# Kernel tuning notes

Measured on AMD Instinct MI355X. Metric: run time of the kernel, lower is better.

The kernel has to match this reference:

```python
import jax, jax.numpy as jnp
import numpy as np

N_DIM = 16
E_DIM = 16
M_DIM = 16
HIDDEN = 64
N_EDGE = 1_600_000
N_NODE = 100_000


def setup_inputs() -> dict:
    key = jax.random.key(0)
    k1, k2, k3, k4, k5, k6, k7 = jax.random.split(key, 7)
    index_v = jax.random.randint(k1, (N_EDGE,), 0, N_NODE, dtype=jnp.int32)
    h_w = jax.random.normal(k2, (N_EDGE, N_DIM), dtype=jnp.float32)
    e_vw = jax.random.normal(k3, (N_EDGE, E_DIM), dtype=jnp.float32)
    # NNet params: Linear(e_dim, hidden) -> ReLU -> Linear(hidden, n_dim*m_dim)
    s1 = 1.0 / np.sqrt(E_DIM)
    s2 = 1.0 / np.sqrt(HIDDEN)
    W1 = jax.random.uniform(k4, (E_DIM, HIDDEN), jnp.float32, -s1, s1)
    b1 = jax.random.uniform(k5, (HIDDEN,), jnp.float32, -s1, s1)
    W2 = jax.random.uniform(k6, (HIDDEN, N_DIM * M_DIM), jnp.float32, -s2, s2)
    b2 = jax.random.uniform(k7, (N_DIM * M_DIM,), jnp.float32, -s2, s2)
    return {"index_v": index_v, "h_w": h_w, "e_vw": e_vw, "n_node": N_NODE,
            "W1": W1, "b1": b1, "W2": W2, "b2": b2}


def reference(index_v, h_w, e_vw, n_node, W1, b1, W2, b2):
    # Edge MLP: [n_edge, e_dim] -> [n_edge, n_dim*m_dim]
    hid = jax.nn.relu(e_vw @ W1 + b1)
    A_vw = (hid @ W2 + b2).reshape(-1, M_DIM, N_DIM)  # [n_edge, m_dim, n_dim]
    # Per-edge matvec: bmm(A_vw, h_w[:, :, None]) -> [n_edge, m_dim]
    m_vw = jnp.einsum("emn,en->em", A_vw, h_w)
    # Scatter-add messages to target nodes: [n_node, m_dim]
    m_v = jax.ops.segment_sum(m_vw, index_v, num_segments=n_node)
    return m_v
```

## Files before the change

### kernel.cpp

```cpp
#include <hip/hip_runtime.h>
#include <stdint.h>

typedef __bf16 bf16x8 __attribute__((ext_vector_type(8)));
typedef float  f32x4  __attribute__((ext_vector_type(4)));
typedef float  fvec4  __attribute__((ext_vector_type(4)));
typedef float  f32x2  __attribute__((ext_vector_type(2)));

#define EDIM   16
#define HIDDEN 64
#define MDIM   16
#define NDIM   16
#define KCHUNKS 32
#define NREP   8
#define WPB    8

__device__ __forceinline__ uint32_t pack_trunc(float x, float y) {
    return __builtin_amdgcn_perm(__builtin_bit_cast(uint32_t, x),
                                 __builtin_bit_cast(uint32_t, y),
                                 0x03020706u);
}

__device__ __forceinline__ uint16_t f32_to_bf16_rne(float f) {
    uint32_t u = __builtin_bit_cast(uint32_t, f);
    u += 0x7FFFu + ((u >> 16) & 1u);
    return (uint16_t)(u >> 16);
}

__device__ __forceinline__ bf16x8 u4_as_bf16x8(uint32_t a, uint32_t b,
                                               uint32_t c, uint32_t d) {
    union { uint32_t u[4]; bf16x8 v; } x;
    x.u[0] = a; x.u[1] = b; x.u[2] = c; x.u[3] = d;
    return x.v;
}

__device__ __forceinline__ f32x2 pk_mul(f32x2 a, f32x2 b) {
    f32x2 d;
    asm("v_pk_mul_f32 %0, %1, %2" : "=v"(d) : "v"(a), "v"(b));
    return d;
}

__device__ __forceinline__ void atomic_add_s(const float* base, uint32_t off,
                                             float v) {
    asm volatile("global_atomic_add_f32 %0, %1, %2"
                 :: "v"(off), "v"(v), "s"(base) : "memory");
}

template<int REPL>
__global__ __launch_bounds__(512, 6) void msg_mfma(
    const int*   __restrict__ idx,
    const float* __restrict__ h_w,
    const float* __restrict__ e_vw,
    const float* __restrict__ W1,
    const float* __restrict__ b1,
    const float* __restrict__ W2,
    const float* __restrict__ b2,
    float*       __restrict__ outb,
    int n_edge, int rep_stride)
{
    __align__(16) __shared__ ushort sB[KCHUNKS * 512];
    __align__(16) __shared__ ushort sHid[WPB * 64 * 16];

    const int tid = threadIdx.x;

    const float* out;
    if (REPL) {
        int xcd = __builtin_amdgcn_s_getreg(6164) & (NREP - 1);
        out = outb + (size_t)xcd * (size_t)rep_stride;
    } else {
        out = outb;
    }

    for (int t = tid; t < KCHUNKS * 512; t += 512) {
        int c = t >> 9, r = t & 511;
        int qq = r >> 7, m = (r >> 3) & 15, j = r & 7;
        int k = 2 * c + (qq >> 1);
        int n = ((qq & 1) << 3) + j;
        sB[t] = f32_to_bf16_rne(W2[k * 256 + m * 16 + n]);
    }

    const int lane = tid & 63;
    const int q    = lane >> 4;
    const int col  = lane & 15;
    const int w    = tid >> 6;

    uint32_t w1u[4][4];
    #pragma unroll
    for (int nt = 0; nt < 4; nt++) {
        #pragma unroll
        for (int d = 0; d < 4; d++) w1u[nt][d] = 0;
        #pragma unroll
        for (int j = 0; j < 8; j++) {
            int k = q * 8 + j;
            float v = 0.f;
            if (k < 16)       v = W1[k * 64 + nt * 16 + col];
            else if (k == 16) v = b1[nt * 16 + col];
            w1u[nt][j >> 1] |= ((uint32_t)f32_to_bf16_rne(v)) << ((j & 1) * 16);
        }
    }

    uint32_t b2u[4] = {0, 0, 0, 0};
    if (q < 2) {
        const float* bp = b2 + col * 16 + q * 8;
        #pragma unroll
        for (int j = 0; j < 8; j++)
            b2u[j >> 1] |= ((uint32_t)f32_to_bf16_rne(bp[j])) << ((j & 1) * 16);
    }
    __syncthreads();

    bf16x8 w1f[4];
    #pragma unroll
    for (int nt = 0; nt < 4; nt++)
        w1f[nt] = u4_as_bf16x8(w1u[nt][0], w1u[nt][1], w1u[nt][2], w1u[nt][3]);
    const bf16x8 b2f = u4_as_bf16x8(b2u[0], b2u[1], b2u[2], b2u[3]);

    const int nhalf = (q & 1) << 3;
    const int ntile = (n_edge + 15) >> 4;
    const int wave_id = blockIdx.x * WPB + w;
    const int wstride = gridDim.x * WPB;
    if (wave_id >= ntile) return;

    const ushort* hidRd = &sHid[w * 1024 + (q >> 1) * 16 + col];
    ushort*       hidWr = &sHid[w * 1024 + col * 16 + q * 4];
    const ushort* bRd   = &sB[q * 128 + col * 8];
    const uint32_t col4 = (uint32_t)col * 4u;

    int t = wave_id;
    fvec4 e0, e1, h0, h1; int4 nd; bool full;
    {
        int rbase = t * 16;
        full = (rbase + 16 <= n_edge);
        int row = full ? (rbase + col) : min(rbase + col, n_edge - 1);
        uint32_t ro = (uint32_t)row * 16u + (uint32_t)nhalf;
        const fvec4* ep = (const fvec4*)(e_vw + ro);
        e0 = __builtin_nontemporal_load(ep);
        e1 = __builtin_nontemporal_load(ep + 1);
        const fvec4* hp = (const fvec4*)(h_w + ro);
        h0 = __builtin_nontemporal_load(hp);
        h1 = __builtin_nontemporal_load(hp + 1);
        int r0 = rbase + q * 4;
        if (full) {
            nd.x = __builtin_nontemporal_load(idx + r0 + 0);
            nd.y = __builtin_nontemporal_load(idx + r0 + 1);
            nd.z = __builtin_nontemporal_load(idx + r0 + 2);
            nd.w = __builtin_nontemporal_load(idx + r0 + 3);
        } else {
            nd.x = __builtin_nontemporal_load(idx + min(r0 + 0, n_edge - 1));
            nd.y = __builtin_nontemporal_load(idx + min(r0 + 1, n_edge - 1));
            nd.z = __builtin_nontemporal_load(idx + min(r0 + 2, n_edge - 1));
            nd.w = __builtin_nontemporal_load(idx + min(r0 + 3, n_edge - 1));
        }
    }

    while (true) {
        int tn = t + wstride;
        bool have_next = (tn < ntile);
        fvec4 ne0, ne1, nh0, nh1; int4 nnd; bool nfull = false;
        if (have_next) {
            int rbase = tn * 16;
            nfull = (rbase + 16 <= n_edge);
            int row = nfull ? (rbase + col) : min(rbase + col, n_edge - 1);
            uint32_t ro = (uint32_t)row * 16u + (uint32_t)nhalf;
            const fvec4* ep = (const fvec4*)(e_vw + ro);
            ne0 = __builtin_nontemporal_load(ep);
            ne1 = __builtin_nontemporal_load(ep + 1);
            const fvec4* hp = (const fvec4*)(h_w + ro);
            nh0 = __builtin_nontemporal_load(hp);
            nh1 = __builtin_nontemporal_load(hp + 1);
            int r0 = rbase + q * 4;
            if (nfull) {
                nnd.x = __builtin_nontemporal_load(idx + r0 + 0);
                nnd.y = __builtin_nontemporal_load(idx + r0 + 1);
                nnd.z = __builtin_nontemporal_load(idx + r0 + 2);
                nnd.w = __builtin_nontemporal_load(idx + r0 + 3);
            } else {
                nnd.x = __builtin_nontemporal_load(idx + min(r0 + 0, n_edge - 1));
                nnd.y = __builtin_nontemporal_load(idx + min(r0 + 1, n_edge - 1));
                nnd.z = __builtin_nontemporal_load(idx + min(r0 + 2, n_edge - 1));
                nnd.w = __builtin_nontemporal_load(idx + min(r0 + 3, n_edge - 1));
            }
        }

        uint32_t au0 = pack_trunc(e0.x, e0.y);
        uint32_t au1 = pack_trunc(e0.z, e0.w);
        uint32_t au2 = pack_trunc(e1.x, e1.y);
        uint32_t au3 = pack_trunc(e1.z, e1.w);
        if (q == 2) { au0 = 0x00003F80u; au1 = au2 = au3 = 0; }
        else if (q == 3) { au0 = au1 = au2 = au3 = 0; }
        bf16x8 av = u4_as_bf16x8(au0, au1, au2, au3);

        #pragma unroll
        for (int nt = 0; nt < 4; nt++) {
            f32x4 hc = {0.f, 0.f, 0.f, 0.f};
            hc = __builtin_amdgcn_mfma_f32_16x16x32_bf16(av, w1f[nt], hc, 0, 0, 0);
            uint32_t lo = pack_trunc(fmaxf(hc[0], 0.f), fmaxf(hc[1], 0.f));
            uint32_t hi = pack_trunc(fmaxf(hc[2], 0.f), fmaxf(hc[3], 0.f));
            *(uint2*)(hidWr + nt * 256) = make_uint2(lo, hi);
        }

        f32x2 hp0; hp0.x = h0.x; hp0.y = h0.y;
        f32x2 hp1; hp1.x = h0.z; hp1.y = h0.w;
        f32x2 hp2; hp2.x = h1.x; hp2.y = h1.y;
        f32x2 hp3; hp3.x = h1.z; hp3.y = h1.w;

        f32x4 acc = {0.f, 0.f, 0.f, 0.f};
        {
            uint32_t a0 = pack_trunc(hp0.x, hp0.y);
            uint32_t a1 = pack_trunc(hp1.x, hp1.y);
            uint32_t a2 = pack_trunc(hp2.x, hp2.y);
            uint32_t a3 = pack_trunc(hp3.x, hp3.y);
            bf16x8 af = u4_as_bf16x8(a0, a1, a2, a3);
            acc = __builtin_amdgcn_mfma_f32_16x16x32_bf16(af, b2f, acc, 0, 0, 0);
        }

        #pragma unroll
        for (int c = 0; c < KCHUNKS; c++) {
            uint32_t hku = ((uint32_t)hidRd[c * 32]) << 16;
            float hkf = __builtin_bit_cast(float, hku);
            f32x2 hk2; hk2.x = hkf; hk2.y = hkf;
            f32x2 p0 = pk_mul(hk2, hp0);
            f32x2 p1 = pk_mul(hk2, hp1);
            f32x2 p2 = pk_mul(hk2, hp2);
            f32x2 p3 = pk_mul(hk2, hp3);
            uint32_t a0 = pack_trunc(p0.x, p0.y);
            uint32_t a1 = pack_trunc(p1.x, p1.y);
            uint32_t a2 = pack_trunc(p2.x, p2.y);
            uint32_t a3 = pack_trunc(p3.x, p3.y);
            bf16x8 af = u4_as_bf16x8(a0, a1, a2, a3);
            bf16x8 bfb = *(const bf16x8*)(bRd + c * 512);
            acc = __builtin_amdgcn_mfma_f32_16x16x32_bf16(af, bfb, acc, 0, 0, 0);
        }

        if (REPL) {
            if (full) {
                atomic_add_s(out, (uint32_t)nd.x * 64u + col4, acc[0]);
                atomic_add_s(out, (uint32_t)nd.y * 64u + col4, acc[1]);
                atomic_add_s(out, (uint32_t)nd.z * 64u + col4, acc[2]);
                atomic_add_s(out, (uint32_t)nd.w * 64u + col4, acc[3]);
            } else {
                int r0 = t * 16 + q * 4;
                if (r0 + 0 < n_edge) atomic_add_s(out, (uint32_t)nd.x * 64u + col4, acc[0]);
                if (r0 + 1 < n_edge) atomic_add_s(out, (uint32_t)nd.y * 64u + col4, acc[1]);
                if (r0 + 2 < n_edge) atomic_add_s(out, (uint32_t)nd.z * 64u + col4, acc[2]);
                if (r0 + 3 < n_edge) atomic_add_s(out, (uint32_t)nd.w * 64u + col4, acc[3]);
            }
        } else {
            float* o = (float*)out;
            int r0 = t * 16 + q * 4;
            if (r0 + 0 < n_edge) atomicAdd(o + (size_t)nd.x * 16 + col, acc[0]);
            if (r0 + 1 < n_edge) atomicAdd(o + (size_t)nd.y * 16 + col, acc[1]);
            if (r0 + 2 < n_edge) atomicAdd(o + (size_t)nd.z * 16 + col, acc[2]);
            if (r0 + 3 < n_edge) atomicAdd(o + (size_t)nd.w * 16 + col, acc[3]);
        }

        if (!have_next) break;
        t = tn;
        e0 = ne0; e1 = ne1; h0 = nh0; h1 = nh1; nd = nnd; full = nfull;
    }
}

__global__ void merge_rep(const fvec4* __restrict__ rep,
                          fvec4* __restrict__ out, int n4, int stride4)
{
    int i = blockIdx.x * blockDim.x + threadIdx.x;
    if (i >= n4) return;
    fvec4 s = rep[i];
    #pragma unroll
    for (int r = 1; r < NREP; r++)
        s += rep[(size_t)r * stride4 + i];
    out[i] = s;
}

extern "C" void kernel_launch(void* const* d_in, const int* in_sizes, int n_in,
                              void* d_out, int out_size, void* d_ws, size_t ws_size,
                              hipStream_t stream) {
    const int*   idx  = (const int*)  d_in[0];
    const float* h_w  = (const float*)d_in[1];
    const float* e_vw = (const float*)d_in[2];
    const float* W1   = (const float*)d_in[4];
    const float* b1   = (const float*)d_in[5];
    const float* W2   = (const float*)d_in[6];
    const float* b2   = (const float*)d_in[7];
    float* out = (float*)d_out;
    const int n_edge = in_sizes[0];

    const size_t out_floats = (size_t)out_size;
    const size_t need = (size_t)NREP * out_floats * sizeof(float);

    if (ws_size >= need && (out_floats & 3) == 0) {
        float* rep = (float*)d_ws;
        hipMemsetAsync(rep, 0, need, stream);
        msg_mfma<1><<<1536, 512, 0, stream>>>(idx, h_w, e_vw, W1, b1, W2, b2,
                                              rep, n_edge, (int)out_floats);
        const int n4 = (int)(out_floats >> 2);
        const int mblocks = (n4 + 255) / 256;
        merge_rep<<<mblocks, 256, 0, stream>>>((const fvec4*)rep, (fvec4*)out,
                                               n4, n4);
    } else {
        hipMemsetAsync(out, 0, out_floats * sizeof(float), stream);
        msg_mfma<0><<<1536, 512, 0, stream>>>(idx, h_w, e_vw, W1, b1, W2, b2,
                                              out, n_edge, 0);
    }
}
```

Measured before the change: 324.6 us.

## Pre-pack W2 bf16 fragments in a global buffer and read via cache instead of LDS

Adds a small prep kernel that converts W2 to bf16 MFMA fragment layout once per call into workspace. The main kernel then loads the B fragments straight from global memory, relying on L1/L2 caching, instead of staging 32KB in LDS. This removes the per-block LDS fill and the barrier, cuts LDS use so occupancy can rise (launch bounds 8, grid 1024). The cost is an extra launch plus global/L1 load latency inside the inner MFMA loop, which may stall compared with LDS reads. The old non-replicated path is kept as a separate legacy kernel.

```diff
diff --git a/kernel.cpp b/kernel.cpp
--- a/kernel.cpp
+++ b/kernel.cpp
@@ -45,38 +45,35 @@
                  :: "v"(off), "v"(v), "s"(base) : "memory");
 }
 
-template<int REPL>
-__global__ __launch_bounds__(512, 6) void msg_mfma(
+__global__ void prep_w2frag(const float* __restrict__ W2,
+                            ushort* __restrict__ w2f)
+{
+    int t = blockIdx.x * blockDim.x + threadIdx.x;
+    if (t >= KCHUNKS * 512) return;
+    int c = t >> 9, r = t & 511;
+    int qq = r >> 7, m = (r >> 3) & 15, j = r & 7;
+    int k = 2 * c + (qq >> 1);
+    int n = ((qq & 1) << 3) + j;
+    w2f[t] = f32_to_bf16_rne(W2[k * 256 + m * 16 + n]);
+}
+
+__global__ __launch_bounds__(512, 8) void msg_mfma_l1(
     const int*   __restrict__ idx,
     const float* __restrict__ h_w,
     const float* __restrict__ e_vw,
     const float* __restrict__ W1,
     const float* __restrict__ b1,
-    const float* __restrict__ W2,
+    const ushort* __restrict__ w2f,
     const float* __restrict__ b2,
     float*       __restrict__ outb,
     int n_edge, int rep_stride)
 {
-    __align__(16) __shared__ ushort sB[KCHUNKS * 512];
     __align__(16) __shared__ ushort sHid[WPB * 64 * 16];
 
     const int tid = threadIdx.x;
 
-    const float* out;
-    if (REPL) {
-        int xcd = __builtin_amdgcn_s_getreg(6164) & (NREP - 1);
-        out = outb + (size_t)xcd * (size_t)rep_stride;
-    } else {
-        out = outb;
-    }
-
-    for (int t = tid; t < KCHUNKS * 512; t += 512) {
-        int c = t >> 9, r = t & 511;
-        int qq = r >> 7, m = (r >> 3) & 15, j = r & 7;
-        int k = 2 * c + (qq >> 1);
-        int n = ((qq & 1) << 3) + j;
-        sB[t] = f32_to_bf16_rne(W2[k * 256 + m * 16 + n]);
-    }
+    const int xcd = __builtin_amdgcn_s_getreg(6164) & (NREP - 1);
+    const float* out = outb + (size_t)xcd * (size_t)rep_stride;
 
     const int lane = tid & 63;
     const int q    = lane >> 4;
@@ -105,7 +102,6 @@
         for (int j = 0; j < 8; j++)
             b2u[j >> 1] |= ((uint32_t)f32_to_bf16_rne(bp[j])) << ((j & 1) * 16);
     }
-    __syncthreads();
 
     bf16x8 w1f[4];
     #pragma unroll
@@ -121,7 +117,7 @@
 
     const ushort* hidRd = &sHid[w * 1024 + (q >> 1) * 16 + col];
     ushort*       hidWr = &sHid[w * 1024 + col * 16 + q * 4];
-    const ushort* bRd   = &sB[q * 128 + col * 8];
+    const bf16x8* bRd = (const bf16x8*)w2f + (q * 16 + col);
     const uint32_t col4 = (uint32_t)col * 4u;
 
     int t = wave_id;
@@ -214,6 +210,7 @@
 
         #pragma unroll
         for (int c = 0; c < KCHUNKS; c++) {
+            bf16x8 bfb = bRd[c * 64];
             uint32_t hku = ((uint32_t)hidRd[c * 32]) << 16;
             float hkf = __builtin_bit_cast(float, hku);
             f32x2 hk2; hk2.x = hkf; hk2.y = hkf;
@@ -226,35 +223,137 @@
             uint32_t a2 = pack_trunc(p2.x, p2.y);
             uint32_t a3 = pack_trunc(p3.x, p3.y);
             bf16x8 af = u4_as_bf16x8(a0, a1, a2, a3);
-            bf16x8 bfb = *(const bf16x8*)(bRd + c * 512);
             acc = __builtin_amdgcn_mfma_f32_16x16x32_bf16(af, bfb, acc, 0, 0, 0);
         }
 
-        if (REPL) {
-            if (full) {
-                atomic_add_s(out, (uint32_t)nd.x * 64u + col4, acc[0]);
-                atomic_add_s(out, (uint32_t)nd.y * 64u + col4, acc[1]);
-                atomic_add_s(out, (uint32_t)nd.z * 64u + col4, acc[2]);
-                atomic_add_s(out, (uint32_t)nd.w * 64u + col4, acc[3]);
-            } else {
-                int r0 = t * 16 + q * 4;
-                if (r0 + 0 < n_edge) atomic_add_s(out, (uint32_t)nd.x * 64u + col4, acc[0]);
-                if (r0 + 1 < n_edge) atomic_add_s(out, (uint32_t)nd.y * 64u + col4, acc[1]);
-                if (r0 + 2 < n_edge) atomic_add_s(out, (uint32_t)nd.z * 64u + col4, acc[2]);
-                if (r0 + 3 < n_edge) atomic_add_s(out, (uint32_t)nd.w * 64u + col4, acc[3]);
-            }
+        if (full) {
+            atomic_add_s(out, (uint32_t)nd.x * 64u + col4, acc[0]);
+            atomic_add_s(out, (uint32_t)nd.y * 64u + col4, acc[1]);
+            atomic_add_s(out, (uint32_t)nd.z * 64u + col4, acc[2]);
+            atomic_add_s(out, (uint32_t)nd.w * 64u + col4, acc[3]);
         } else {
-            float* o = (float*)out;
             int r0 = t * 16 + q * 4;
-            if (r0 + 0 < n_edge) atomicAdd(o + (size_t)nd.x * 16 + col, acc[0]);
-            if (r0 + 1 < n_edge) atomicAdd(o + (size_t)nd.y * 16 + col, acc[1]);
-            if (r0 + 2 < n_edge) atomicAdd(o + (size_t)nd.z * 16 + col, acc[2]);
-            if (r0 + 3 < n_edge) atomicAdd(o + (size_t)nd.w * 16 + col, acc[3]);
+            if (r0 + 0 < n_edge) atomic_add_s(out, (uint32_t)nd.x * 64u + col4, acc[0]);
+            if (r0 + 1 < n_edge) atomic_add_s(out, (uint32_t)nd.y * 64u + col4, acc[1]);
+            if (r0 + 2 < n_edge) atomic_add_s(out, (uint32_t)nd.z * 64u + col4, acc[2]);
+            if (r0 + 3 < n_edge) atomic_add_s(out, (uint32_t)nd.w * 64u + col4, acc[3]);
         }
 
         if (!have_next) break;
         t = tn;
         e0 = ne0; e1 = ne1; h0 = nh0; h1 = nh1; nd = nnd; full = nfull;
+    }
+}
+
+__global__ __launch_bounds__(512, 6) void msg_mfma_legacy(
+    const int*   __restrict__ idx,
+    const float* __restrict__ h_w,
+    const float* __restrict__ e_vw,
+    const float* __restrict__ W1,
+    const float* __restrict__ b1,
+    const float* __restrict__ W2,
+    const float* __restrict__ b2,
+    float*       __restrict__ out,
+    int n_edge)
+{
+    __align__(16) __shared__ ushort sB[KCHUNKS * 512];
+    __align__(16) __shared__ ushort sHid[WPB * 64 * 16];
+    const int tid = threadIdx.x;
+    for (int t = tid; t < KCHUNKS * 512; t += 512) {
+        int c = t >> 9, r = t & 511;
+        int qq = r >> 7, m = (r >> 3) & 15, j = r & 7;
+        int k = 2 * c + (qq >> 1);
+        int n = ((qq & 1) << 3) + j;
+        sB[t] = f32_to_bf16_rne(W2[k * 256 + m * 16 + n]);
+    }
+    const int lane = tid & 63, q = lane >> 4, col = lane & 15, w = tid >> 6;
+    uint32_t w1u[4][4];
+    #pragma unroll
+    for (int nt = 0; nt < 4; nt++) {
+        #pragma unroll
+        for (int d = 0; d < 4; d++) w1u[nt][d] = 0;
+        #pragma unroll
+        for (int j = 0; j < 8; j++) {
+            int k = q * 8 + j;
+            float v = 0.f;
+            if (k < 16)       v = W1[k * 64 + nt * 16 + col];
+            else if (k == 16) v = b1[nt * 16 + col];
+            w1u[nt][j >> 1] |= ((uint32_t)f32_to_bf16_rne(v)) << ((j & 1) * 16);
+        }
+    }
+    uint32_t b2u[4] = {0, 0, 0, 0};
+    if (q < 2) {
+        const float* bp = b2 + col * 16 + q * 8;
+        #pragma unroll
+        for (int j = 0; j < 8; j++)
+            b2u[j >> 1] |= ((uint32_t)f32_to_bf16_rne(bp[j])) << ((j & 1) * 16);
+    }
+    __syncthreads();
+    bf16x8 w1f[4];
+    #pragma unroll
+    for (int nt = 0; nt < 4; nt++)
+        w1f[nt] = u4_as_bf16x8(w1u[nt][0], w1u[nt][1], w1u[nt][2], w1u[nt][3]);
+    const bf16x8 b2f = u4_as_bf16x8(b2u[0], b2u[1], b2u[2], b2u[3]);
+    const int nhalf = (q & 1) << 3;
+    const int ntile = (n_edge + 15) >> 4;
+    int t = blockIdx.x * WPB + w;
+    const int wstride = gridDim.x * WPB;
+    const ushort* hidRd = &sHid[w * 1024 + (q >> 1) * 16 + col];
+    ushort*       hidWr = &sHid[w * 1024 + col * 16 + q * 4];
+    const ushort* bRd   = &sB[q * 128 + col * 8];
+    for (; t < ntile; t += wstride) {
+        int row = min(t * 16 + col, n_edge - 1);
+        const fvec4* ep = (const fvec4*)(e_vw + (size_t)row * 16 + nhalf);
+        fvec4 e0 = ep[0], e1 = ep[1];
+        const fvec4* hpp = (const fvec4*)(h_w + (size_t)row * 16 + nhalf);
+        fvec4 h0 = hpp[0], h1 = hpp[1];
+        int r0 = t * 16 + q * 4;
+        int4 nd;
+        nd.x = idx[min(r0 + 0, n_edge - 1)];
+        nd.y = idx[min(r0 + 1, n_edge - 1)];
+        nd.z = idx[min(r0 + 2, n_edge - 1)];
+        nd.w = idx[min(r0 + 3, n_edge - 1)];
+        uint32_t au0 = pack_trunc(e0.x, e0.y);
+        uint32_t au1 = pack_trunc(e0.z, e0.w);
+        uint32_t au2 = pack_trunc(e1.x, e1.y);
+        uint32_t au3 = pack_trunc(e1.z, e1.w);
+        if (q == 2) { au0 = 0x00003F80u; au1 = au2 = au3 = 0; }
+        else if (q == 3) { au0 = au1 = au2 = au3 = 0; }
+        bf16x8 av = u4_as_bf16x8(au0, au1, au2, au3);
+        #pragma unroll
+        for (int nt = 0; nt < 4; nt++) {
+            f32x4 hc = {0.f, 0.f, 0.f, 0.f};
+            hc = __builtin_amdgcn_mfma_f32_16x16x32_bf16(av, w1f[nt], hc, 0, 0, 0);
+            uint32_t lo = pack_trunc(fmaxf(hc[0], 0.f), fmaxf(hc[1], 0.f));
+            uint32_t hi = pack_trunc(fmaxf(hc[2], 0.f), fmaxf(hc[3], 0.f));
+            *(uint2*)(hidWr + nt * 256) = make_uint2(lo, hi);
+        }
+        float hf[8] = {h0.x, h0.y, h0.z, h0.w, h1.x, h1.y, h1.z, h1.w};
+        f32x4 acc = {0.f, 0.f, 0.f, 0.f};
+        {
+            uint32_t a0 = pack_trunc(hf[0], hf[1]);
+            uint32_t a1 = pack_trunc(hf[2], hf[3]);
+            uint32_t a2 = pack_trunc(hf[4], hf[5]);
+            uint32_t a3 = pack_trunc(hf[6], hf[7]);
+            acc = __builtin_amdgcn_mfma_f32_16x16x32_bf16(
+                u4_as_bf16x8(a0, a1, a2, a3), b2f, acc, 0, 0, 0);
+        }
+        #pragma unroll
+        for (int c = 0; c < KCHUNKS; c++) {
+            uint32_t hku = ((uint32_t)hidRd[c * 32]) << 16;
+            float hk = __builtin_bit_cast(float, hku);
+            uint32_t a0 = pack_trunc(hk * hf[0], hk * hf[1]);
+            uint32_t a1 = pack_trunc(hk * hf[2], hk * hf[3]);
+            uint32_t a2 = pack_trunc(hk * hf[4], hk * hf[5]);
+            uint32_t a3 = pack_trunc(hk * hf[6], hk * hf[7]);
+            bf16x8 bfb = *(const bf16x8*)(bRd + c * 512);
+            acc = __builtin_amdgcn_mfma_f32_16x16x32_bf16(
+                u4_as_bf16x8(a0, a1, a2, a3), bfb, acc, 0, 0, 0);
+        }
+        if (r0 + 0 < n_edge) atomicAdd(out + (size_t)nd.x * 16 + col, acc[0]);
+        if (r0 + 1 < n_edge) atomicAdd(out + (size_t)nd.y * 16 + col, acc[1]);
+        if (r0 + 2 < n_edge) atomicAdd(out + (size_t)nd.z * 16 + col, acc[2]);
+        if (r0 + 3 < n_edge) atomicAdd(out + (size_t)nd.w * 16 + col, acc[3]);
     }
 }
 
@@ -284,12 +383,16 @@
     const int n_edge = in_sizes[0];
 
     const size_t out_floats = (size_t)out_size;
-    const size_t need = (size_t)NREP * out_floats * sizeof(float);
+    const size_t need_rep = (size_t)NREP * out_floats * sizeof(float);
+    const size_t w2off = (need_rep + 255) & ~(size_t)255;
+    const size_t need = w2off + (size_t)KCHUNKS * 512 * sizeof(ushort);
 
     if (ws_size >= need && (out_floats & 3) == 0) {
-        float* rep = (float*)d_ws;
-        hipMemsetAsync(rep, 0, need, stream);
-        msg_mfma<1><<<1536, 512, 0, stream>>>(idx, h_w, e_vw, W1, b1, W2, b2,
+        float*  rep = (float*)d_ws;
+        ushort* w2f = (ushort*)((char*)d_ws + w2off);
+        hipMemsetAsync(rep, 0, need_rep, stream);
+        prep_w2frag<<<32, 512, 0, stream>>>(W2, w2f);
+        msg_mfma_l1<<<1024, 512, 0, stream>>>(idx, h_w, e_vw, W1, b1, w2f, b2,
                                               rep, n_edge, (int)out_floats);
         const int n4 = (int)(out_floats >> 2);
         const int mblocks = (n4 + 255) / 256;
@@ -297,7 +400,7 @@
                                                n4, n4);
     } else {
         hipMemsetAsync(out, 0, out_floats * sizeof(float), stream);
-        msg_mfma<0><<<1536, 512, 0, stream>>>(idx, h_w, e_vw, W1, b1, W2, b2,
-                                              out, n_edge, 0);
-    }
-}
+        msg_mfma_legacy<<<1536, 512, 0, stream>>>(idx, h_w, e_vw, W1, b1, W2,
+                                                  b2, out, n_edge);
+    }
+}
```

New measurement: 655.8 us. 102% more time.
